# Kernel tuning notes

Measured on AMD Instinct MI355X. Metric: run time of the kernel, lower is better.

The kernel has to match this reference:

```python
import jax, jax.numpy as jnp
import numpy as np


def setup_inputs() -> dict:
    key = jax.random.key(0)
    k1, k2, k3, k4, k5 = jax.random.split(key, 5)
    B, L1, L2, H = 16, 1024, 1024, 1024
    x = jax.random.normal(k1, (B, L1, H), dtype=jnp.float32)
    y = jax.random.normal(k2, (B, L2, H), dtype=jnp.float32)
    y_mask = jax.random.randint(k3, (B, L2), 0, 2) > 0  # True = masked out
    W = jax.random.normal(k4, (H, H), dtype=jnp.float32) * (1.0 / np.sqrt(H))
    b = jax.random.normal(k5, (H,), dtype=jnp.float32) * 0.01
    return {"x": x, "y": y, "y_mask": y_mask, "W": W, "b": b}


def reference(x, y, y_mask, W, b):
    # shared linear projection + ReLU (nn.Linear: v @ W.T + b)
    x_proj = jax.nn.relu(jnp.einsum("blh,dh->bld", x, W) + b)  # [B, L1, H]
    y_proj = jax.nn.relu(jnp.einsum("bmh,dh->bmd", y, W) + b)  # [B, L2, H]
    # unscaled attention scores [B, L1, L2]
    scores = jnp.einsum("bld,bmd->blm", x_proj, y_proj)
    scores = jnp.where(y_mask[:, None, :], -jnp.inf, scores)
    alpha = jax.nn.softmax(scores, axis=-1)
    # weighted sum over original (unprojected) y values
    matched_seq = jnp.einsum("blm,bmh->blh", alpha, y)
    return matched_seq
```

## Files before the change

kernel.cpp:

```cpp
#include <hip/hip_runtime.h>
#include <hip/hip_fp16.h>

typedef _Float16 f16;
typedef _Float16 half4 __attribute__((ext_vector_type(4)));
typedef _Float16 half8 __attribute__((ext_vector_type(8)));
typedef float f32x4 __attribute__((ext_vector_type(4)));

#define BATCH 16
#define L 1024
#define H 1024

__global__ __launch_bounds__(256) void cvt_wx(const float* __restrict__ W,
                                              f16* __restrict__ Wh,
                                              const float* __restrict__ x,
                                              f16* __restrict__ Xh) {
  const float* src;
  f16* dst;
  long i;
  if (blockIdx.x < 512) {
    src = W; dst = Wh;
    i = (long)blockIdx.x * 2048 + threadIdx.x * 8;
  } else {
    src = x; dst = Xh;
    i = ((long)blockIdx.x - 512) * 2048 + threadIdx.x * 8;
  }
  const float4 a = *(const float4*)(&src[i]);
  const float4 b = *(const float4*)(&src[i + 4]);
  half8 h;
  h[0] = (f16)a.x; h[1] = (f16)a.y; h[2] = (f16)a.z; h[3] = (f16)a.w;
  h[4] = (f16)b.x; h[5] = (f16)b.y; h[6] = (f16)b.z; h[7] = (f16)b.w;
  *(half8*)(&dst[i]) = h;
}

__global__ __launch_bounds__(256) void mask_scan(const int* __restrict__ mask,
                                                 int* __restrict__ posx,
                                                 int* __restrict__ cntA) {
  const int b = blockIdx.x;
  const int t = threadIdx.x;
  const int4 mk = *(const int4*)(&mask[b * 1024 + t * 4]);
  const int f0 = (mk.x == 0), f1 = (mk.y == 0);
  const int f2 = (mk.z == 0), f3 = (mk.w == 0);
  const int s = f0 + f1 + f2 + f3;
  int v = s;
  const int lane = t & 63, wd = t >> 6;
  #pragma unroll
  for (int off = 1; off < 64; off <<= 1) {
    const int u = __shfl_up(v, off);
    if (lane >= off) v += u;
  }
  __shared__ int wsum[4];
  if (lane == 63) wsum[wd] = v;
  __syncthreads();
  int wb = 0;
  #pragma unroll
  for (int k = 0; k < 3; ++k)
    if (k < wd) wb += wsum[k];
  int e = wb + v - s;
  const int base = b * 1024 + t * 4;
  posx[base + 0] = e; e += f0;
  posx[base + 1] = e; e += f1;
  posx[base + 2] = e; e += f2;
  posx[base + 3] = e; e += f3;
  if (t == 255) cntA[b] = e;
}

__global__ void offsets_k(const int* __restrict__ cntA, int* __restrict__ off17) {
  if (threadIdx.x == 0) {
    int a = 0;
    off17[0] = 0;
    for (int b = 0; b < 16; ++b) { a += cntA[b]; off17[b + 1] = a; }
  }
}

__global__ __launch_bounds__(256) void transpose_y(
    const float* __restrict__ Y, const int* __restrict__ mask,
    const int* __restrict__ posx, const int* __restrict__ cntA,
    const int* __restrict__ off17, f16* __restrict__ Yhc,
    f16* __restrict__ Ytc) {
  __shared__ f16 tile[64][36];
  __shared__ int cmap[32];
  const int b = blockIdx.z;
  const int h0 = blockIdx.x * 64, m0 = blockIdx.y * 32;
  const int tid = threadIdx.x;
  const float* Yb = Y + (long)b * L * H;
  f16* Ytb = Ytc + (long)b * L * H;

  const int jbase = posx[b * 1024 + m0];
  const int cnt = cntA[b];
  const int nloc = ((m0 == L - 32) ? cnt : posx[b * 1024 + m0 + 32]) - jbase;
  const int rowbase = off17[b];

  const int hc = (tid & 15) * 4;
  #pragma unroll
  for (int rr = 0; rr < 2; ++rr) {
    const int m = (tid >> 4) + rr * 16;
    const int gm = b * 1024 + m0 + m;
    const int jc = posx[gm];
    const int un = (mask[gm] == 0);
    const float4 v = *(const float4*)(&Yb[(long)(m0 + m) * H + h0 + hc]);
    half4 h4;
    h4[0] = (f16)v.x; h4[1] = (f16)v.y; h4[2] = (f16)v.z; h4[3] = (f16)v.w;
    tile[hc + 0][m] = h4[0];
    tile[hc + 1][m] = h4[1];
    tile[hc + 2][m] = h4[2];
    tile[hc + 3][m] = h4[3];
    if (un) {
      *(half4*)(&Yhc[(long)(rowbase + jc) * H + h0 + hc]) = h4;
      if (hc == 0) cmap[jc - jbase] = m;
    }
  }
  __syncthreads();
  {
    const int c = tid & 31;
    if (c < nloc) {
      const int m = cmap[c];
      for (int hh = tid >> 5; hh < 64; hh += 8)
        Ytb[(long)(h0 + hh) * L + jbase + c] = tile[hh][m];
    }
  }
  if (m0 == L - 32) {
    const int p = ((cnt + 31) & ~31) - cnt;
    const int c = tid & 31;
    if (c < p)
      for (int hh = tid >> 5; hh < 64; hh += 8)
        Ytb[(long)(h0 + hh) * L + cnt + c] = (f16)0.f;
  }
}

#define GLD16(g, l)                                           \
  __builtin_amdgcn_global_load_lds(                           \
      (const __attribute__((address_space(1))) void*)(g),     \
      (__attribute__((address_space(3))) void*)(l), 16, 0, 0)

template <int MODE>
__global__ __launch_bounds__(512, 4) void gemm128(
    const f16* __restrict__ Ap, const f16* __restrict__ Bp,
    const float* __restrict__ bias, void* __restrict__ Cp,
    const int* __restrict__ off17, int nxyShift) {
  __shared__ f16 lds[3 * 12288];
  constexpr int N = 1024, K = 1024;

  const int tid = threadIdx.x;
  const int lane = tid & 63;
  const int wid = tid >> 6;
  const int wm = wid >> 1;
  const int wn = wid & 1;

  const int nwg = gridDim.x;
  const int orig = blockIdx.x;
  const int wg = (orig & 7) * (nwg >> 3) + (orig >> 3);
  const int bz = wg >> nxyShift;
  const int rxy = wg & ((1 << nxyShift) - 1);
  const int bx = rxy & 7;
  const int by = rxy >> 3;
  const int row0 = by * 256, col0 = bx * 128;

  const int srow = lane >> 2;
  const int sslot = (lane & 3) ^ ((lane >> 3) & 3);

  int nt = 32;
  const f16 *gA0, *gA1, *gB0;
  if (MODE == 0) {
    const int total = off17[16];
    if (row0 >= 16384 + total + 32) return;
    gA0 = Ap + (long)(row0 + wid * 32 + srow) * K + sslot * 8;
    gA1 = gA0 + 16L * K;
    gB0 = Bp + (long)(col0 + wid * 16 + srow) * K + sslot * 8;
  } else if (MODE == 1) {
    const int cnt = off17[bz + 1] - off17[bz];
    if (col0 >= ((cnt + 31) & ~31)) return;
    gA0 = Ap + (long)(bz * 1024 + row0 + wid * 32 + srow) * K + sslot * 8;
    gA1 = gA0 + 16L * K;
    gB0 = Ap + (long)(16384 + off17[bz] + col0 + wid * 16 + srow) * K +
          sslot * 8;
  } else {
    const int cnt = off17[bz + 1] - off17[bz];
    nt = ((cnt + 31) & ~31) >> 5;
    gA0 = Ap + (long)bz * (1 << 20) +
          (long)(row0 + wid * 32 + srow) * 1024 + sslot * 8;
    gA1 = gA0 + 16L * 1024;
    gB0 = Bp + (long)bz * (1 << 20) +
          (long)(col0 + wid * 16 + srow) * 1024 + sslot * 8;
  }
  char* ldsw = (char*)lds;

  const int fr = lane & 15, fq = lane >> 4;
  const int rsw = (fq ^ ((fr >> 1) & 3)) << 4;
  const int aByte = (wm * 64 + fr) * 64 + rsw;
  const int bByte = (wn * 64 + fr) * 64 + rsw;
  const char* ldsr = (const char*)lds;

  f32x4 acc[4][4];
  #pragma unroll
  for (int i = 0; i < 4; ++i)
    #pragma unroll
    for (int j = 0; j < 4; ++j)
      acc[i][j] = (f32x4){0.f, 0.f, 0.f, 0.f};

  #pragma unroll
  for (int p = 0; p < 2; ++p) {
    char* sb = ldsw + p * 24576;
    GLD16(gA0, sb + wid * 2048);
    GLD16(gA1, sb + wid * 2048 + 1024);
    GLD16(gB0, sb + 16384 + wid * 1024);
    gA0 += 32; gA1 += 32; gB0 += 32;
  }
  asm volatile("s_waitcnt vmcnt(3)" ::: "memory");
  __builtin_amdgcn_s_barrier();
  __builtin_amdgcn_sched_barrier(0);

  int cb = 0, pb = 2 * 24576;
  const int NT = (MODE == 2) ? nt : 32;
  for (int t = 0; t < NT; ++t) {
    if (t + 2 < NT) {
      char* sb = ldsw + pb;
      GLD16(gA0, sb + wid * 2048);
      GLD16(gA1, sb + wid * 2048 + 1024);
      GLD16(gB0, sb + 16384 + wid * 1024);
      gA0 += 32; gA1 += 32; gB0 += 32;
    }
    const char* base = ldsr + cb;
    half8 av[4], bv[4];
    #pragma unroll
    for (int j = 0; j < 4; ++j)
      bv[j] = *(const half8*)(base + 16384 + bByte + j * 1024);
    #pragma unroll
    for (int i = 0; i < 4; ++i)
      av[i] = *(const half8*)(base + aByte + i * 1024);
    __builtin_amdgcn_s_setprio(1);
    #pragma unroll
    for (int i = 0; i < 4; ++i)
      #pragma unroll
      for (int j = 0; j < 4; ++j)
        acc[i][j] = __builtin_amdgcn_mfma_f32_16x16x32_f16(av[i], bv[j],
                                                           acc[i][j], 0, 0, 0);
    __builtin_amdgcn_s_setprio(0);
    if (t < NT - 1) {
      __builtin_amdgcn_sched_barrier(0);
      if (t <= NT - 3)
        asm volatile("s_waitcnt vmcnt(3)" ::: "memory");
      else
        asm volatile("s_waitcnt vmcnt(0)" ::: "memory");
      __builtin_amdgcn_s_barrier();
      __builtin_amdgcn_sched_barrier(0);
      cb = (cb == 49152) ? 0 : cb + 24576;
      pb = (pb == 49152) ? 0 : pb + 24576;
    }
  }

  if (MODE == 0) {
    f16* C = (f16*)Cp;
    #pragma unroll
    for (int j = 0; j < 4; ++j) {
      const int col = col0 + wn * 64 + j * 16 + fr;
      const float bvs = bias[col];
      #pragma unroll
      for (int i = 0; i < 4; ++i) {
        const int rowb = row0 + wm * 64 + i * 16 + fq * 4;
        #pragma unroll
        for (int r = 0; r < 4; ++r) {
          float v = acc[i][j][r] + bvs;
          v = v > 0.f ? v : 0.f;
          C[(long)(rowb + r) * N + col] = (f16)v;
        }
      }
    }
  } else {
    float* C = (float*)Cp + (long)bz * (1 << 20);
    #pragma unroll
    for (int j = 0; j < 4; ++j) {
      const int col = col0 + wn * 64 + j * 16 + fr;
      #pragma unroll
      for (int i = 0; i < 4; ++i) {
        const int rowb = row0 + wm * 64 + i * 16 + fq * 4;
        #pragma unroll
        for (int r = 0; r < 4; ++r)
          C[(long)(rowb + r) * N + col] = acc[i][j][r];
      }
    }
  }
}

__global__ __launch_bounds__(256) void softmax_rows(const float* __restrict__ S,
                                                    const int* __restrict__ off17,
                                                    f16* __restrict__ P) {
  const int b = blockIdx.y;
  const int l = blockIdx.x;
  const int t = threadIdx.x;
  const int cnt = off17[b + 1] - off17[b];
  const int cnt32 = (cnt + 31) & ~31;
  const float* srow = S + ((long)b * L + l) * L;
  f16* prow = P + ((long)b * L + l) * L;

  const float4 v = *(const float4*)(&srow[t * 4]);
  const int j0 = t * 4;
  const float x0 = (j0 + 0 < cnt) ? v.x : -1e30f;
  const float x1 = (j0 + 1 < cnt) ? v.y : -1e30f;
  const float x2 = (j0 + 2 < cnt) ? v.z : -1e30f;
  const float x3 = (j0 + 3 < cnt) ? v.w : -1e30f;

  float mx = fmaxf(fmaxf(x0, x1), fmaxf(x2, x3));
  #pragma unroll
  for (int off = 32; off >= 1; off >>= 1)
    mx = fmaxf(mx, __shfl_xor(mx, off));
  __shared__ float red[8];
  const int wd = t >> 6, lane = t & 63;
  if (lane == 0) red[wd] = mx;
  __syncthreads();
  mx = fmaxf(fmaxf(red[0], red[1]), fmaxf(red[2], red[3]));

  const float e0 = __expf(x0 - mx), e1 = __expf(x1 - mx);
  const float e2 = __expf(x2 - mx), e3 = __expf(x3 - mx);
  float s = e0 + e1 + e2 + e3;
  #pragma unroll
  for (int off = 32; off >= 1; off >>= 1)
    s += __shfl_xor(s, off);
  if (lane == 0) red[4 + wd] = s;
  __syncthreads();
  s = red[4] + red[5] + red[6] + red[7];
  const float inv = 1.f / s;
  if (j0 < cnt32) {
    half4 h;
    h[0] = (f16)(e0 * inv); h[1] = (f16)(e1 * inv);
    h[2] = (f16)(e2 * inv); h[3] = (f16)(e3 * inv);
    *(half4*)(&prow[j0]) = h;
  }
}

extern "C" void kernel_launch(void* const* d_in, const int* in_sizes, int n_in,
                              void* d_out, int out_size, void* d_ws,
                              size_t ws_size, hipStream_t stream) {
  const float* x = (const float*)d_in[0];
  const float* y = (const float*)d_in[1];
  const int* ymask = (const int*)d_in[2];
  const float* W = (const float*)d_in[3];
  const float* bias = (const float*)d_in[4];
  float* out = (float*)d_out;

  char* ws = (char*)d_ws;
  f16* Wh = (f16*)(ws);
  f16* Ytc = (f16*)(ws + (1L << 21));
  f16* XYp = (f16*)(ws + (1L << 21) + (1L << 25));
  f16* XYh = (f16*)(ws + (1L << 21) + (1L << 25) + (1L << 26));
  float* Sc = (float*)XYh;
  f16* Alpha = XYp;

  char* meta = (char*)XYp + 60L * (1 << 20);
  int* posx = (int*)meta;
  int* cntA = (int*)(meta + (1 << 16));
  int* off17 = (int*)(meta + (1 << 16) + 256);

  f16* Xh = XYh;
  f16* Yhc = XYh + (long)BATCH * L * H;

  cvt_wx<<<512 + 8192, 256, 0, stream>>>(W, Wh, x, Xh);
  mask_scan<<<16, 256, 0, stream>>>(ymask, posx, cntA);
  offsets_k<<<1, 64, 0, stream>>>(cntA, off17);
  transpose_y<<<dim3(16, 32, BATCH), 256, 0, stream>>>(y, ymask, posx, cntA,
                                                       off17, Yhc, Ytc);

  gemm128<0><<<1024, 512, 0, stream>>>(XYh, Wh, bias, XYp, off17, 10);

  gemm128<1><<<512, 512, 0, stream>>>(XYp, nullptr, nullptr, Sc, off17, 5);

  softmax_rows<<<dim3(L, BATCH), 256, 0, stream>>>(Sc, off17, Alpha);

  gemm128<2><<<512, 512, 0, stream>>>(Alpha, Ytc, nullptr, out, off17, 5);
}
```

Measured before the change: 201.8 us.

## Merge prep kernels, drop offsets kernel, use persistent atomic tile scheduler for projection

```diff
diff --git a/kernel.cpp b/kernel.cpp
--- a/kernel.cpp
+++ b/kernel.cpp
@@ -10,33 +10,37 @@
 #define L 1024
 #define H 1024
 
-__global__ __launch_bounds__(256) void cvt_wx(const float* __restrict__ W,
-                                              f16* __restrict__ Wh,
-                                              const float* __restrict__ x,
-                                              f16* __restrict__ Xh) {
-  const float* src;
-  f16* dst;
-  long i;
-  if (blockIdx.x < 512) {
-    src = W; dst = Wh;
-    i = (long)blockIdx.x * 2048 + threadIdx.x * 8;
-  } else {
-    src = x; dst = Xh;
-    i = ((long)blockIdx.x - 512) * 2048 + threadIdx.x * 8;
-  }
-  const float4 a = *(const float4*)(&src[i]);
-  const float4 b = *(const float4*)(&src[i + 4]);
-  half8 h;
-  h[0] = (f16)a.x; h[1] = (f16)a.y; h[2] = (f16)a.z; h[3] = (f16)a.w;
-  h[4] = (f16)b.x; h[5] = (f16)b.y; h[6] = (f16)b.z; h[7] = (f16)b.w;
-  *(half8*)(&dst[i]) = h;
-}
-
-__global__ __launch_bounds__(256) void mask_scan(const int* __restrict__ mask,
-                                                 int* __restrict__ posx,
-                                                 int* __restrict__ cntA) {
-  const int b = blockIdx.x;
+__global__ __launch_bounds__(256) void prep(const float* __restrict__ W,
+                                            f16* __restrict__ Wh,
+                                            const float* __restrict__ x,
+                                            f16* __restrict__ Xh,
+                                            const int* __restrict__ mask,
+                                            int* __restrict__ posx,
+                                            int* __restrict__ cntA,
+                                            int* __restrict__ tileCtr) {
+  __shared__ int wsum[4];
   const int t = threadIdx.x;
+  if (blockIdx.x < 8704) {
+    const float* src;
+    f16* dst;
+    long i;
+    if (blockIdx.x < 512) {
+      src = W; dst = Wh;
+      i = (long)blockIdx.x * 2048 + t * 8;
+    } else {
+      src = x; dst = Xh;
+      i = ((long)blockIdx.x - 512) * 2048 + t * 8;
+    }
+    const float4 a = *(const float4*)(&src[i]);
+    const float4 b = *(const float4*)(&src[i + 4]);
+    half8 h;
+    h[0] = (f16)a.x; h[1] = (f16)a.y; h[2] = (f16)a.z; h[3] = (f16)a.w;
+    h[4] = (f16)b.x; h[5] = (f16)b.y; h[6] = (f16)b.z; h[7] = (f16)b.w;
+    *(half8*)(&dst[i]) = h;
+    return;
+  }
+  const int b = blockIdx.x - 8704;
+  if (b == 0 && t == 0) tileCtr[0] = 0;
   const int4 mk = *(const int4*)(&mask[b * 1024 + t * 4]);
   const int f0 = (mk.x == 0), f1 = (mk.y == 0);
   const int f2 = (mk.z == 0), f3 = (mk.w == 0);
@@ -48,7 +52,6 @@
     const int u = __shfl_up(v, off);
     if (lane >= off) v += u;
   }
-  __shared__ int wsum[4];
   if (lane == 63) wsum[wd] = v;
   __syncthreads();
   int wb = 0;
@@ -64,19 +67,10 @@
   if (t == 255) cntA[b] = e;
 }
 
-__global__ void offsets_k(const int* __restrict__ cntA, int* __restrict__ off17) {
-  if (threadIdx.x == 0) {
-    int a = 0;
-    off17[0] = 0;
-    for (int b = 0; b < 16; ++b) { a += cntA[b]; off17[b + 1] = a; }
-  }
-}
-
 __global__ __launch_bounds__(256) void transpose_y(
     const float* __restrict__ Y, const int* __restrict__ mask,
     const int* __restrict__ posx, const int* __restrict__ cntA,
-    const int* __restrict__ off17, f16* __restrict__ Yhc,
-    f16* __restrict__ Ytc) {
+    f16* __restrict__ Yhc, f16* __restrict__ Ytc) {
   __shared__ f16 tile[64][36];
   __shared__ int cmap[32];
   const int b = blockIdx.z;
@@ -85,10 +79,13 @@
   const float* Yb = Y + (long)b * L * H;
   f16* Ytb = Ytc + (long)b * L * H;
 
+  int rowbase = 0;
+  #pragma unroll
+  for (int k = 0; k < 16; ++k)
+    if (k < b) rowbase += cntA[k];
   const int jbase = posx[b * 1024 + m0];
   const int cnt = cntA[b];
   const int nloc = ((m0 == L - 32) ? cnt : posx[b * 1024 + m0 + 32]) - jbase;
-  const int rowbase = off17[b];
 
   const int hc = (tid & 15) * 4;
   #pragma unroll
@@ -132,124 +129,93 @@
       (const __attribute__((address_space(1))) void*)(g),     \
       (__attribute__((address_space(3))) void*)(l), 16, 0, 0)
 
-template <int MODE>
-__global__ __launch_bounds__(512, 4) void gemm128(
-    const f16* __restrict__ Ap, const f16* __restrict__ Bp,
-    const float* __restrict__ bias, void* __restrict__ Cp,
-    const int* __restrict__ off17, int nxyShift) {
+#define GEMM_PIPELINE(NTv)                                                   \
+  f32x4 acc[4][4];                                                           \
+  _Pragma("unroll") for (int i = 0; i < 4; ++i)                              \
+      _Pragma("unroll") for (int j = 0; j < 4; ++j)                          \
+          acc[i][j] = (f32x4){0.f, 0.f, 0.f, 0.f};                           \
+  _Pragma("unroll") for (int p = 0; p < 2; ++p) {                            \
+    char* sb = ldsw + p * 24576;                                             \
+    GLD16(gA0, sb + wid * 2048);                                             \
+    GLD16(gA1, sb + wid * 2048 + 1024);                                      \
+    GLD16(gB0, sb + 16384 + wid * 1024);                                     \
+    gA0 += 32; gA1 += 32; gB0 += 32;                                         \
+  }                                                                          \
+  asm volatile("s_waitcnt vmcnt(3)" ::: "memory");                           \
+  __builtin_amdgcn_s_barrier();                                              \
+  __builtin_amdgcn_sched_barrier(0);                                         \
+  int cb = 0, pb = 2 * 24576;                                                \
+  for (int t = 0; t < NTv; ++t) {                                            \
+    if (t + 2 < NTv) {                                                       \
+      char* sb = ldsw + pb;                                                  \
+      GLD16(gA0, sb + wid * 2048);                                           \
+      GLD16(gA1, sb + wid * 2048 + 1024);                                    \
+      GLD16(gB0, sb + 16384 + wid * 1024);                                   \
+      gA0 += 32; gA1 += 32; gB0 += 32;                                       \
+    }                                                                        \
+    const char* base = ldsr + cb;                                            \
+    half8 av[4], bv[4];                                                      \
+    _Pragma("unroll") for (int j = 0; j < 4; ++j)                            \
+        bv[j] = *(const half8*)(base + 16384 + bByte + j * 1024);            \
+    _Pragma("unroll") for (int i = 0; i < 4; ++i)                            \
+        av[i] = *(const half8*)(base + aByte + i * 1024);                    \
+    __builtin_amdgcn_s_setprio(1);                                           \
+    _Pragma("unroll") for (int i = 0; i < 4; ++i)                            \
+        _Pragma("unroll") for (int j = 0; j < 4; ++j)                        \
+            acc[i][j] = __builtin_amdgcn_mfma_f32_16x16x32_f16(              \
+                av[i], bv[j], acc[i][j], 0, 0, 0);                           \
+    __builtin_amdgcn_s_setprio(0);                                           \
+    if (t < NTv - 1) {                                                       \
+      __builtin_amdgcn_sched_barrier(0);                                     \
+      if (t <= NTv - 3)                                                      \
+        asm volatile("s_waitcnt vmcnt(3)" ::: "memory");                     \
+      else                                                                   \
+        asm volatile("s_waitcnt vmcnt(0)" ::: "memory");                     \
+      __builtin_amdgcn_s_barrier();                                          \
+      __builtin_amdgcn_sched_barrier(0);                                     \
+      cb = (cb == 49152) ? 0 : cb + 24576;                                   \
+      pb = (pb == 49152) ? 0 : pb + 24576;                                   \
+    }                                                                        \
+  }
+
+__global__ __launch_bounds__(512, 4) void gemm_proj(
+    const f16* __restrict__ Ap, const f16* __restrict__ Wp,
+    const float* __restrict__ bias, f16* __restrict__ Cp,
+    const int* __restrict__ cntA, int* __restrict__ tileCtr) {
   __shared__ f16 lds[3 * 12288];
+  __shared__ int sTile;
   constexpr int N = 1024, K = 1024;
-
   const int tid = threadIdx.x;
   const int lane = tid & 63;
   const int wid = tid >> 6;
-  const int wm = wid >> 1;
-  const int wn = wid & 1;
-
-  const int nwg = gridDim.x;
-  const int orig = blockIdx.x;
-  const int wg = (orig & 7) * (nwg >> 3) + (orig >> 3);
-  const int bz = wg >> nxyShift;
-  const int rxy = wg & ((1 << nxyShift) - 1);
-  const int bx = rxy & 7;
-  const int by = rxy >> 3;
-  const int row0 = by * 256, col0 = bx * 128;
+  const int wm = wid >> 1, wn = wid & 1;
+  int total = 0;
+  #pragma unroll
+  for (int k = 0; k < 16; ++k) total += cntA[k];
+  const int Ntiles = ((16384 + total + 32 + 255) >> 8) << 3;
 
   const int srow = lane >> 2;
   const int sslot = (lane & 3) ^ ((lane >> 3) & 3);
-
-  int nt = 32;
-  const f16 *gA0, *gA1, *gB0;
-  if (MODE == 0) {
-    const int total = off17[16];
-    if (row0 >= 16384 + total + 32) return;
-    gA0 = Ap + (long)(row0 + wid * 32 + srow) * K + sslot * 8;
-    gA1 = gA0 + 16L * K;
-    gB0 = Bp + (long)(col0 + wid * 16 + srow) * K + sslot * 8;
-  } else if (MODE == 1) {
-    const int cnt = off17[bz + 1] - off17[bz];
-    if (col0 >= ((cnt + 31) & ~31)) return;
-    gA0 = Ap + (long)(bz * 1024 + row0 + wid * 32 + srow) * K + sslot * 8;
-    gA1 = gA0 + 16L * K;
-    gB0 = Ap + (long)(16384 + off17[bz] + col0 + wid * 16 + srow) * K +
-          sslot * 8;
-  } else {
-    const int cnt = off17[bz + 1] - off17[bz];
-    nt = ((cnt + 31) & ~31) >> 5;
-    gA0 = Ap + (long)bz * (1 << 20) +
-          (long)(row0 + wid * 32 + srow) * 1024 + sslot * 8;
-    gA1 = gA0 + 16L * 1024;
-    gB0 = Bp + (long)bz * (1 << 20) +
-          (long)(col0 + wid * 16 + srow) * 1024 + sslot * 8;
-  }
-  char* ldsw = (char*)lds;
-
   const int fr = lane & 15, fq = lane >> 4;
   const int rsw = (fq ^ ((fr >> 1) & 3)) << 4;
   const int aByte = (wm * 64 + fr) * 64 + rsw;
   const int bByte = (wn * 64 + fr) * 64 + rsw;
+  char* ldsw = (char*)lds;
   const char* ldsr = (const char*)lds;
 
-  f32x4 acc[4][4];
-  #pragma unroll
-  for (int i = 0; i < 4; ++i)
-    #pragma unroll
-    for (int j = 0; j < 4; ++j)
-      acc[i][j] = (f32x4){0.f, 0.f, 0.f, 0.f};
-
-  #pragma unroll
-  for (int p = 0; p < 2; ++p) {
-    char* sb = ldsw + p * 24576;
-    GLD16(gA0, sb + wid * 2048);
-    GLD16(gA1, sb + wid * 2048 + 1024);
-    GLD16(gB0, sb + 16384 + wid * 1024);
-    gA0 += 32; gA1 += 32; gB0 += 32;
-  }
-  asm volatile("s_waitcnt vmcnt(3)" ::: "memory");
-  __builtin_amdgcn_s_barrier();
-  __builtin_amdgcn_sched_barrier(0);
-
-  int cb = 0, pb = 2 * 24576;
-  const int NT = (MODE == 2) ? nt : 32;
-  for (int t = 0; t < NT; ++t) {
-    if (t + 2 < NT) {
-      char* sb = ldsw + pb;
-      GLD16(gA0, sb + wid * 2048);
-      GLD16(gA1, sb + wid * 2048 + 1024);
-      GLD16(gB0, sb + 16384 + wid * 1024);
-      gA0 += 32; gA1 += 32; gB0 += 32;
-    }
-    const char* base = ldsr + cb;
-    half8 av[4], bv[4];
-    #pragma unroll
-    for (int j = 0; j < 4; ++j)
-      bv[j] = *(const half8*)(base + 16384 + bByte + j * 1024);
-    #pragma unroll
-    for (int i = 0; i < 4; ++i)
-      av[i] = *(const half8*)(base + aByte + i * 1024);
-    __builtin_amdgcn_s_setprio(1);
-    #pragma unroll
-    for (int i = 0; i < 4; ++i)
-      #pragma unroll
-      for (int j = 0; j < 4; ++j)
-        acc[i][j] = __builtin_amdgcn_mfma_f32_16x16x32_f16(av[i], bv[j],
-                                                           acc[i][j], 0, 0, 0);
-    __builtin_amdgcn_s_setprio(0);
-    if (t < NT - 1) {
-      __builtin_amdgcn_sched_barrier(0);
-      if (t <= NT - 3)
-        asm volatile("s_waitcnt vmcnt(3)" ::: "memory");
-      else
-        asm volatile("s_waitcnt vmcnt(0)" ::: "memory");
-      __builtin_amdgcn_s_barrier();
-      __builtin_amdgcn_sched_barrier(0);
-      cb = (cb == 49152) ? 0 : cb + 24576;
-      pb = (pb == 49152) ? 0 : pb + 24576;
-    }
-  }
-
-  if (MODE == 0) {
-    f16* C = (f16*)Cp;
+  while (true) {
+    if (tid == 0) sTile = atomicAdd(tileCtr, 1);
+    __syncthreads();
+    const int tile = sTile;
+    if (tile >= Ntiles) return;
+    const int row0 = (tile >> 3) * 256, col0 = (tile & 7) * 128;
+    const f16* gA0 = Ap + (long)(row0 + wid * 32 + srow) * K + sslot * 8;
+    const f16* gA1 = gA0 + 16L * K;
+    const f16* gB0 = Wp + (long)(col0 + wid * 16 + srow) * K + sslot * 8;
+
+    GEMM_PIPELINE(32)
+
+    f16* C = Cp;
     #pragma unroll
     for (int j = 0; j < 4; ++j) {
       const int col = col0 + wn * 64 + j * 16 + fr;
@@ -265,35 +231,94 @@
         }
       }
     }
+    __syncthreads();
+  }
+}
+
+template <int MODE>
+__global__ __launch_bounds__(512, 4) void gemm128(
+    const f16* __restrict__ Ap, const f16* __restrict__ Bp,
+    void* __restrict__ Cp, const int* __restrict__ cntA) {
+  __shared__ f16 lds[3 * 12288];
+  constexpr int N = 1024, K = 1024;
+  const int tid = threadIdx.x;
+  const int lane = tid & 63;
+  const int wid = tid >> 6;
+  const int wm = wid >> 1, wn = wid & 1;
+
+  const int nwg = gridDim.x;
+  const int orig = blockIdx.x;
+  const int wg = (orig & 7) * (nwg >> 3) + (orig >> 3);
+  const int bz = wg >> 5;
+  const int rxy = wg & 31;
+  const int bx = rxy & 7;
+  const int by = rxy >> 3;
+  const int row0 = by * 256, col0 = bx * 128;
+
+  int off = 0;
+  #pragma unroll
+  for (int k = 0; k < 16; ++k)
+    if (k < bz) off += cntA[k];
+  const int cnt = cntA[bz];
+  const int cnt32 = (cnt + 31) & ~31;
+
+  const int srow = lane >> 2;
+  const int sslot = (lane & 3) ^ ((lane >> 3) & 3);
+
+  int nt = 32;
+  const f16 *gA0, *gA1, *gB0;
+  if (MODE == 1) {
+    if (col0 >= cnt32) return;
+    gA0 = Ap + (long)(bz * 1024 + row0 + wid * 32 + srow) * K + sslot * 8;
+    gA1 = gA0 + 16L * K;
+    gB0 = Ap + (long)(16384 + off + col0 + wid * 16 + srow) * K + sslot * 8;
   } else {
-    float* C = (float*)Cp + (long)bz * (1 << 20);
+    nt = cnt32 >> 5;
+    gA0 = Ap + (long)bz * (1 << 20) +
+          (long)(row0 + wid * 32 + srow) * 1024 + sslot * 8;
+    gA1 = gA0 + 16L * 1024;
+    gB0 = Bp + (long)bz * (1 << 20) +
+          (long)(col0 + wid * 16 + srow) * 1024 + sslot * 8;
+  }
+  char* ldsw = (char*)lds;
+
+  const int fr = lane & 15, fq = lane >> 4;
+  const int rsw = (fq ^ ((fr >> 1) & 3)) << 4;
+  const int aByte = (wm * 64 + fr) * 64 + rsw;
+  const int bByte = (wn * 64 + fr) * 64 + rsw;
+  const char* ldsr = (const char*)lds;
+
+  const int NT = (MODE == 2) ? nt : 32;
+  GEMM_PIPELINE(NT)
+
+  float* C = (float*)Cp + (long)bz * (1 << 20);
+  #pragma unroll
+  for (int j = 0; j < 4; ++j) {
+    const int col = col0 + wn * 64 + j * 16 + fr;
     #pragma unroll
-    for (int j = 0; j < 4; ++j) {
-      const int col = col0 + wn * 64 + j * 16 + fr;
+    for (int i = 0; i < 4; ++i) {
+      const int rowb = row0 + wm * 64 + i * 16 + fq * 4;
       #pragma unroll
-      for (int i = 0; i < 4; ++i) {
-        const int rowb = row0 + wm * 64 + i * 16 + fq * 4;
-        #pragma unroll
-        for (int r = 0; r < 4; ++r)
-          C[(long)(rowb + r) * N + col] = acc[i][j][r];
-      }
+      for (int r = 0; r < 4; ++r)
+        C[(long)(rowb + r) * N + col] = acc[i][j][r];
     }
   }
 }
 
 __global__ __launch_bounds__(256) void softmax_rows(const float* __restrict__ S,
-                                                    const int* __restrict__ off17,
+                                                    const int* __restrict__ cntA,
                                                     f16* __restrict__ P) {
   const int b = blockIdx.y;
   const int l = blockIdx.x;
   const int t = threadIdx.x;
-  const int cnt = off17[b + 1] - off17[b];
+  const int cnt = cntA[b];
   const int cnt32 = (cnt + 31) & ~31;
   const float* srow = S + ((long)b * L + l) * L;
   f16* prow = P + ((long)b * L + l) * L;
 
-  const float4 v = *(const float4*)(&srow[t * 4]);
   const int j0 = t * 4;
+  float4 v = make_float4(-1e30f, -1e30f, -1e30f, -1e30f);
+  if (j0 < cnt32) v = *(const float4*)(&srow[j0]);
   const float x0 = (j0 + 0 < cnt) ? v.x : -1e30f;
   const float x1 = (j0 + 1 < cnt) ? v.y : -1e30f;
   const float x2 = (j0 + 2 < cnt) ? v.z : -1e30f;
@@ -348,22 +373,21 @@
   char* meta = (char*)XYp + 60L * (1 << 20);
   int* posx = (int*)meta;
   int* cntA = (int*)(meta + (1 << 16));
-  int* off17 = (int*)(meta + (1 << 16) + 256);
+  int* tileCtr = (int*)(meta + (1 << 16) + 256);
 
   f16* Xh = XYh;
   f16* Yhc = XYh + (long)BATCH * L * H;
 
-  cvt_wx<<<512 + 8192, 256, 0, stream>>>(W, Wh, x, Xh);
-  mask_scan<<<16, 256, 0, stream>>>(ymask, posx, cntA);
-  offsets_k<<<1, 64, 0, stream>>>(cntA, off17);
+  prep<<<8704 + 16, 256, 0, stream>>>(W, Wh, x, Xh, ymask, posx, cntA,
+                                      tileCtr);
   transpose_y<<<dim3(16, 32, BATCH), 256, 0, stream>>>(y, ymask, posx, cntA,
-                                                       off17, Yhc, Ytc);
-
-  gemm128<0><<<1024, 512, 0, stream>>>(XYh, Wh, bias, XYp, off17, 10);
-
-  gemm128<1><<<512, 512, 0, stream>>>(XYp, nullptr, nullptr, Sc, off17, 5);
-
-  softmax_rows<<<dim3(L, BATCH), 256, 0, stream>>>(Sc, off17, Alpha);
-
-  gemm128<2><<<512, 512, 0, stream>>>(Alpha, Ytc, nullptr, out, off17, 5);
-}
+                                                       Yhc, Ytc);
+
+  gemm_proj<<<512, 512, 0, stream>>>(XYh, Wh, bias, XYp, cntA, tileCtr);
+
+  gemm128<1><<<512, 512, 0, stream>>>(XYp, nullptr, Sc, cntA);
+
+  softmax_rows<<<dim3(L, BATCH), 256, 0, stream>>>(Sc, cntA, Alpha);
+
+  gemm128<2><<<512, 512, 0, stream>>>(Alpha, Ytc, out, cntA);
+}
```

Result: slower. 205.9 us (+2.0%).
